# Performance work log

Hardware: AMD Instinct MI355X
Metric: run time of the kernel (lower is better)

## Reference

```python
import jax, jax.numpy as jnp
import numpy as np

S, N, F = 32, 512, 256        # systems, atoms per system, feature/charge channels
R_EXCL = 5.0                  # neighbor_list_options.cutoff -> exclusion_radius
BOX = 30.0                    # box edge for random positions (Angstrom-scale)


def setup_inputs() -> dict:
    key = jax.random.key(0)
    k1, k2, k3, k4 = jax.random.split(key, 4)
    positions = jax.random.uniform(k1, (S, N, 3), dtype=jnp.float32) * BOX
    features = jax.random.normal(k2, (S * N, F), dtype=jnp.float32)
    W = jax.random.normal(k3, (F, F), dtype=jnp.float32) / jnp.sqrt(F)
    b = jax.random.normal(k4, (F,), dtype=jnp.float32) * 0.01
    return {"positions": positions, "features": features, "W": W, "b": b}


def _pair_potential(d):
    # CoulombPotential(smearing=None, exclusion_radius=R_EXCL).from_dist:
    # v(r) = (1/r) * (1 - f_cut(r)),  f_cut = 0.5*(1 + cos(pi*r/R_EXCL)) for r < R_EXCL
    fcut = jnp.where(d < R_EXCL, 0.5 * (1.0 + jnp.cos(jnp.pi * d / R_EXCL)), 0.0)
    return (1.0 / d) * (1.0 - fcut)


def reference(positions, features, W, b):
    # charges_map: Linear(F, F)
    charges = features @ W.T + b                      # [S*N, F]
    q = charges.reshape(S, N, F)                      # per-system charges

    # all-pairs distances per system (torch.combinations path, both directions
    # accumulated by the half-neighbor-list Calculator)
    diff = positions[:, :, None, :] - positions[:, None, :, :]   # [S,N,N,3]
    d = jnp.sqrt(jnp.sum(diff * diff, axis=-1))                  # [S,N,N]
    eye = jnp.eye(N, dtype=bool)
    d_safe = jnp.where(eye, 1.0, d)
    v = jnp.where(eye, 0.0, _pair_potential(d_safe))             # [S,N,N]

    # V_i = 0.5 * sum_j v(r_ij) q_j  (torchpme energy convention E = sum_i q_i V_i)
    V = 0.5 * jnp.einsum('sij,sjf->sif', v, q)                   # [S,N,F]

    # module returns potential * charges, concatenated over systems
    return (V * q).reshape(S * N, F)
```

## Files before the change

### kernel.cpp

```cpp
#include <hip/hip_runtime.h>
#include <hip/hip_cooperative_groups.h>

#define SY 32
#define NA 512
#define FD 256

typedef __attribute__((ext_vector_type(8))) short bf16x8;
typedef __attribute__((ext_vector_type(4))) short bf16x4;
typedef __attribute__((ext_vector_type(4))) float f32x4;

static __device__ __forceinline__ short f2bf(float x) {
    union { float f; unsigned u; } v; v.f = x;
    unsigned r = v.u + 0x7fffu + ((v.u >> 16) & 1u);
    return (short)(r >> 16);
}
static __device__ __forceinline__ float bf2f(short x) {
    union { float f; unsigned u; } v;
    v.u = ((unsigned)(unsigned short)x) << 16;
    return v.f;
}

static __device__ __forceinline__ void gld16(const void* g, void* l) {
    __builtin_amdgcn_global_load_lds(
        (const __attribute__((address_space(1))) void*)g,
        (__attribute__((address_space(3))) void*)l,
        16, 0, 0);
}

__global__ __launch_bounds__(512) void charges_mfma(
    const float* __restrict__ feat, const float* __restrict__ W,
    const float* __restrict__ b, float* __restrict__ qfp,
    short* __restrict__ qT)
{
    __shared__ __attribute__((aligned(16))) short sA[64 * 72];
    __shared__ __attribute__((aligned(16))) short sB[256 * 72];
    __shared__ __attribute__((aligned(16))) short tr[256 * 72];
    const int t    = threadIdx.x;
    const int i0   = blockIdx.x * 64;
    const int w    = t >> 6;
    const int lane = t & 63;
    const int n16  = lane & 15;
    const int quad = lane >> 4;

    f32x4 acc[4][2];
    #pragma unroll
    for (int a = 0; a < 4; ++a)
        #pragma unroll
        for (int c = 0; c < 2; ++c) acc[a][c] = (f32x4)0.0f;

    for (int k0 = 0; k0 < FD; k0 += 64) {
        #pragma unroll
        for (int m = 0; m < 2; ++m) {
            int lin = t + 512 * m;
            int i = lin >> 4, kq = lin & 15;
            float4 v = *(const float4*)&feat[(size_t)(i0 + i) * FD + k0 + 4 * kq];
            bf16x4 p; p[0] = f2bf(v.x); p[1] = f2bf(v.y);
                      p[2] = f2bf(v.z); p[3] = f2bf(v.w);
            *(bf16x4*)&sA[i * 72 + 4 * kq] = p;
        }
        #pragma unroll
        for (int m = 0; m < 8; ++m) {
            int lin = t + 512 * m;
            int f = lin >> 4, kq = lin & 15;
            float4 v = *(const float4*)&W[(size_t)f * FD + k0 + 4 * kq];
            bf16x4 p; p[0] = f2bf(v.x); p[1] = f2bf(v.y);
                      p[2] = f2bf(v.z); p[3] = f2bf(v.w);
            *(bf16x4*)&sB[f * 72 + 4 * kq] = p;
        }
        __syncthreads();

        #pragma unroll
        for (int ks = 0; ks < 64; ks += 32) {
            bf16x8 af[4], bfr[2];
            #pragma unroll
            for (int it = 0; it < 4; ++it)
                af[it] = *(const bf16x8*)&sA[(16 * it + n16) * 72 + ks + quad * 8];
            #pragma unroll
            for (int fb = 0; fb < 2; ++fb)
                bfr[fb] = *(const bf16x8*)&sB[(32 * w + 16 * fb + n16) * 72 + ks + quad * 8];
            #pragma unroll
            for (int it = 0; it < 4; ++it)
                #pragma unroll
                for (int fb = 0; fb < 2; ++fb)
                    acc[it][fb] = __builtin_amdgcn_mfma_f32_16x16x32_bf16(
                        af[it], bfr[fb], acc[it][fb], 0, 0, 0);
        }
        __syncthreads();
    }

    float bias[2];
    #pragma unroll
    for (int fb = 0; fb < 2; ++fb) bias[fb] = b[32 * w + 16 * fb + n16];

    if (qfp) {
        #pragma unroll
        for (int it = 0; it < 4; ++it)
            #pragma unroll
            for (int fb = 0; fb < 2; ++fb)
                #pragma unroll
                for (int r = 0; r < 4; ++r) {
                    int i = i0 + 16 * it + 4 * quad + r;
                    int f = 32 * w + 16 * fb + n16;
                    qfp[(size_t)i * FD + f] = acc[it][fb][r] + bias[fb];
                }
    }

    #pragma unroll
    for (int it = 0; it < 4; ++it)
        #pragma unroll
        for (int fb = 0; fb < 2; ++fb) {
            bf16x4 p;
            #pragma unroll
            for (int r = 0; r < 4; ++r) p[r] = f2bf(acc[it][fb][r] + bias[fb]);
            int f = 32 * w + 16 * fb + n16;
            *(bf16x4*)&tr[f * 72 + 16 * it + 4 * quad] = p;
        }
    __syncthreads();
    {
        short* qTs = qT + ((size_t)(i0 >> 9)) * FD * NA;
        const int ilb = i0 & 511;
        #pragma unroll
        for (int n = 0; n < 4; ++n) {
            int S = n * 512 + t;
            int f = S >> 3;
            int c = S & 7;
            uint4 v = *(const uint4*)&tr[f * 72 + c * 8];
            *(uint4*)&qTs[(size_t)f * NA + ilb + c * 8] = v;
        }
    }
}

__global__ __launch_bounds__(256, 2) void lr_fast(
    const float* __restrict__ pos, float* __restrict__ gbuf,
    const short* __restrict__ qT)
{
    __shared__ float px[NA], py[NA], pz[NA];
    __shared__ __attribute__((aligned(16))) short sqb[FD * 128];
    __shared__ __attribute__((aligned(16))) short svb[32 * 128];

    const int blk = blockIdx.x;
    const int s   = blk & 31;
    const int i0  = (blk >> 5) * 32;
    const int t   = threadIdx.x;
    const int w    = t >> 6;
    const int lane = t & 63;
    const int n16  = lane & 15;
    const int quad = lane >> 4;

    for (int m = t; m < NA; m += 256) {
        const float* p = &pos[((size_t)s * NA + m) * 3];
        px[m] = p[0]; py[m] = p[1]; pz[m] = p[2];
    }

    f32x4 acc[2][4];
    #pragma unroll
    for (int a = 0; a < 2; ++a)
        #pragma unroll
        for (int c = 0; c < 4; ++c) acc[a][c] = (f32x4)0.0f;
    float qreg[2][4][4];

    const short* qTs = qT + (size_t)s * FD * NA;
    const int pi = t & 31;
    const int pc = t >> 5;
    const int gi = i0 + pi;
    const int wbase = t & ~63;

    __syncthreads();
    const float xi = px[gi], yi = py[gi], zi = pz[gi];

    for (int j0 = 0; j0 < NA; j0 += 128) {
        #pragma unroll
        for (int n = 0; n < 16; ++n) {
            int Sl = n * 256 + t;
            int f  = Sl >> 4;
            int cs = Sl & 15;
            int c  = (cs - f) & 15;
            gld16(&qTs[(size_t)f * NA + j0 + c * 8],
                  &sqb[(n * 256 + wbase) * 8]);
        }
        bf16x8 vA, vB;
        #pragma unroll
        for (int jj = 0; jj < 8; ++jj) {
            int gj = j0 + pc * 16 + jj;
            float dx = xi - px[gj];
            float dy = yi - py[gj];
            float dz = zi - pz[gj];
            float r2 = dx * dx + dy * dy + dz * dz;
            float inv = __builtin_amdgcn_rsqf(r2);
            float dd  = r2 * inv;
            float sn = __sinf(dd * 0.31415926535f);
            float om = (dd < 5.0f) ? sn * sn : 1.0f;
            float vv = (gi != gj) ? 0.5f * om * inv : 0.0f;
            vA[jj] = f2bf(vv);
        }
        #pragma unroll
        for (int jj = 0; jj < 8; ++jj) {
            int gj = j0 + pc * 16 + 8 + jj;
            float dx = xi - px[gj];
            float dy = yi - py[gj];
            float dz = zi - pz[gj];
            float r2 = dx * dx + dy * dy + dz * dz;
            float inv = __builtin_amdgcn_rsqf(r2);
            float dd  = r2 * inv;
            float sn = __sinf(dd * 0.31415926535f);
            float om = (dd < 5.0f) ? sn * sn : 1.0f;
            float vv = (gi != gj) ? 0.5f * om * inv : 0.0f;
            vB[jj] = f2bf(vv);
        }
        *(bf16x8*)&svb[pi * 128 + (((2 * pc + pi) & 15) * 8)]     = vA;
        *(bf16x8*)&svb[pi * 128 + (((2 * pc + 1 + pi) & 15) * 8)] = vB;
        __syncthreads();

        if (j0 == (i0 & ~127)) {
            const int jb0 = i0 & 127;
            #pragma unroll
            for (int it = 0; it < 2; ++it)
                #pragma unroll
                for (int fb = 0; fb < 4; ++fb) {
                    int f = 64 * w + 16 * fb + n16;
                    #pragma unroll
                    for (int r = 0; r < 4; ++r) {
                        int jl = jb0 + 16 * it + 4 * quad + r;
                        int c  = jl >> 3, o = jl & 7;
                        qreg[it][fb][r] =
                            bf2f(sqb[f * 128 + (((c + f) & 15) * 8) + o]);
                    }
                }
        }

        #pragma unroll
        for (int kh = 0; kh < 4; ++kh) {
            const int c = kh * 4 + quad;
            bf16x8 a0 = *(const bf16x8*)&svb[n16 * 128 + (((c + n16) & 15) * 8)];
            bf16x8 a1 = *(const bf16x8*)&svb[(16 + n16) * 128 + (((c + 16 + n16) & 15) * 8)];
            bf16x8 bq[4];
            #pragma unroll
            for (int fb = 0; fb < 4; ++fb) {
                int f = 64 * w + 16 * fb + n16;
                bq[fb] = *(const bf16x8*)&sqb[f * 128 + (((c + f) & 15) * 8)];
            }
            #pragma unroll
            for (int fb = 0; fb < 4; ++fb) {
                acc[0][fb] = __builtin_amdgcn_mfma_f32_16x16x32_bf16(
                    a0, bq[fb], acc[0][fb], 0, 0, 0);
                acc[1][fb] = __builtin_amdgcn_mfma_f32_16x16x32_bf16(
                    a1, bq[fb], acc[1][fb], 0, 0, 0);
            }
        }
        __syncthreads();
    }

    #pragma unroll
    for (int it = 0; it < 2; ++it)
        #pragma unroll
        for (int fb = 0; fb < 4; ++fb)
            #pragma unroll
            for (int r = 0; r < 4; ++r) {
                int i = i0 + 16 * it + 4 * quad + r;
                int f = 64 * w + 16 * fb + n16;
                size_t a = ((size_t)s * NA + i) * FD + f;
                gbuf[a] = acc[it][fb][r] * qreg[it][fb][r];
            }
}

__global__ __launch_bounds__(256) void lr_coop(
    const float* __restrict__ pos, float* __restrict__ gbuf)
{
    __shared__ float px[NA], py[NA], pz[NA];
    __shared__ __attribute__((aligned(16))) short svb[64 * 40];
    __shared__ __attribute__((aligned(16))) short sqb[FD * 40];

    const int blk = blockIdx.x;
    const int s   = blk & 31;
    const int i0  = (blk >> 5) * 64;
    const int t   = threadIdx.x;
    const int w    = t >> 6;
    const int lane = t & 63;
    const int n16  = lane & 15;
    const int quad = lane >> 4;

    for (int m = t; m < NA; m += 256) {
        const float* p = &pos[((size_t)s * NA + m) * 3];
        px[m] = p[0]; py[m] = p[1]; pz[m] = p[2];
    }

    f32x4 acc[4][4];
    #pragma unroll
    for (int a = 0; a < 4; ++a)
        #pragma unroll
        for (int c = 0; c < 4; ++c) acc[a][c] = (f32x4)0.0f;

    __syncthreads();

    const int fq  = t >> 2;
    const int jb  = t & 3;
    const int iv  = t & 63;
    const int jbv = t >> 6;
    const int gi  = i0 + iv;

    float4 rq[8];
    #pragma unroll
    for (int m = 0; m < 8; ++m)
        rq[m] = *(const float4*)&gbuf[((size_t)s * NA + 8 * jb + m) * FD + 4 * fq];

    for (int j0 = 0; j0 < NA; j0 += 32) {
        bf16x8 vrow;
        #pragma unroll
        for (int jj = 0; jj < 8; ++jj) {
            int gj = j0 + 8 * jbv + jj;
            float dx = px[gi] - px[gj];
            float dy = py[gi] - py[gj];
            float dz = pz[gi] - pz[gj];
            float dd = sqrtf(dx * dx + dy * dy + dz * dz);
            float om = (dd < 5.0f) ? 0.5f * (1.0f - __cosf(dd * 0.62831853071795f))
                                   : 1.0f;
            float vv = (gi != gj) ? (0.5f * om * __builtin_amdgcn_rcpf(dd)) : 0.0f;
            vrow[jj] = f2bf(vv);
        }
        bf16x8 rows[4];
        #pragma unroll
        for (int m = 0; m < 8; ++m) {
            rows[0][m] = f2bf(rq[m].x);
            rows[1][m] = f2bf(rq[m].y);
            rows[2][m] = f2bf(rq[m].z);
            rows[3][m] = f2bf(rq[m].w);
        }
        #pragma unroll
        for (int d = 0; d < 4; ++d) {
            int f = 4 * fq + d;
            int phys = (jb + (f >> 3)) & 3;
            *(bf16x8*)&sqb[f * 40 + phys * 8] = rows[d];
        }
        {
            int phys = (jbv + (iv >> 3)) & 3;
            *(bf16x8*)&svb[iv * 40 + phys * 8] = vrow;
        }
        {
            int jn = (j0 + 32) & (NA - 1);
            #pragma unroll
            for (int m = 0; m < 8; ++m)
                rq[m] = *(const float4*)&gbuf[((size_t)s * NA + jn + 8 * jb + m) * FD + 4 * fq];
        }
        __syncthreads();

        bf16x8 af[4], bfr[4];
        #pragma unroll
        for (int it = 0; it < 4; ++it) {
            int i = 16 * it + n16;
            int phys = (quad + (i >> 3)) & 3;
            af[it] = *(const bf16x8*)&svb[i * 40 + phys * 8];
        }
        #pragma unroll
        for (int fb = 0; fb < 4; ++fb) {
            int f = 16 * (4 * w + fb) + n16;
            int phys = (quad + (f >> 3)) & 3;
            bfr[fb] = *(const bf16x8*)&sqb[f * 40 + phys * 8];
        }
        #pragma unroll
        for (int it = 0; it < 4; ++it)
            #pragma unroll
            for (int fb = 0; fb < 4; ++fb)
                acc[it][fb] = __builtin_amdgcn_mfma_f32_16x16x32_bf16(
                    af[it], bfr[fb], acc[it][fb], 0, 0, 0);
        __syncthreads();
    }

    cooperative_groups::this_grid().sync();

    #pragma unroll
    for (int it = 0; it < 4; ++it)
        #pragma unroll
        for (int fb = 0; fb < 4; ++fb)
            #pragma unroll
            for (int r = 0; r < 4; ++r) {
                int i = i0 + 16 * it + 4 * quad + r;
                int f = 16 * (4 * w + fb) + n16;
                size_t a = ((size_t)s * NA + i) * FD + f;
                gbuf[a] = acc[it][fb][r] * gbuf[a];
            }
}

extern "C" void kernel_launch(void* const* d_in, const int* in_sizes, int n_in,
                              void* d_out, int out_size, void* d_ws, size_t ws_size,
                              hipStream_t stream) {
    const float* positions = (const float*)d_in[0];
    const float* features  = (const float*)d_in[1];
    const float* W         = (const float*)d_in[2];
    const float* b         = (const float*)d_in[3];
    float* gbuf = (float*)d_out;

    const size_t qT_bytes = (size_t)SY * NA * FD * sizeof(short);
    const bool fast = (ws_size >= qT_bytes);
    short* qT = fast ? (short*)d_ws : nullptr;

    if (fast) {
        charges_mfma<<<dim3(256), 512, 0, stream>>>(features, W, b, nullptr, qT);
        lr_fast<<<dim3(512), 256, 0, stream>>>(positions, gbuf, qT);
    } else {
        charges_mfma<<<dim3(256), 512, 0, stream>>>(features, W, b, gbuf,
                                                    (short*)d_out );
        void* args[] = {(void*)&positions, (void*)&gbuf};
        hipLaunchCooperativeKernel((void*)lr_coop, dim3(256), dim3(256),
                                   args, 0, stream);
    }
}
```

Baseline: 97.00 us.

## Keep bf16 charges in the output buffer and add a software grid barrier

Drops the workspace and cooperative fallback paths. The transposed bf16 charges now live in the upper half of the output buffer, and lr_fast uses an atomic-counter spin barrier, with a spin limit, before overwriting the output. The charges kernel is retiled to 32-row blocks at 256 threads with 2 blocks per CU and reuses its staging LDS for the transpose. MFMA sections are wrapped in s_setprio. The barrier assumes all 512 blocks are co-resident, and the counter word sits in the output itself. If blocks are not co-resident, the spin times out and the result can be wrong.

```diff
diff --git a/kernel.cpp b/kernel.cpp
--- a/kernel.cpp
+++ b/kernel.cpp
@@ -1,5 +1,4 @@
 #include <hip/hip_runtime.h>
-#include <hip/hip_cooperative_groups.h>
 
 #define SY 32
 #define NA 512
@@ -27,31 +26,34 @@
         16, 0, 0);
 }
 
-__global__ __launch_bounds__(512) void charges_mfma(
+__global__ __launch_bounds__(256, 2) void charges_v2(
     const float* __restrict__ feat, const float* __restrict__ W,
-    const float* __restrict__ b, float* __restrict__ qfp,
-    short* __restrict__ qT)
+    const float* __restrict__ b, short* __restrict__ qT,
+    unsigned* __restrict__ ctr)
 {
-    __shared__ __attribute__((aligned(16))) short sA[64 * 72];
+    __shared__ __attribute__((aligned(16))) short sA[32 * 72];
     __shared__ __attribute__((aligned(16))) short sB[256 * 72];
-    __shared__ __attribute__((aligned(16))) short tr[256 * 72];
+    short* tr = sB;
     const int t    = threadIdx.x;
-    const int i0   = blockIdx.x * 64;
+    const int i0   = blockIdx.x * 32;
     const int w    = t >> 6;
     const int lane = t & 63;
     const int n16  = lane & 15;
     const int quad = lane >> 4;
 
-    f32x4 acc[4][2];
-    #pragma unroll
-    for (int a = 0; a < 4; ++a)
-        #pragma unroll
-        for (int c = 0; c < 2; ++c) acc[a][c] = (f32x4)0.0f;
+    if (blockIdx.x == 0 && t == 0)
+        __hip_atomic_store(ctr, 0u, __ATOMIC_RELAXED, __HIP_MEMORY_SCOPE_AGENT);
+
+    f32x4 acc[2][4];
+    #pragma unroll
+    for (int a = 0; a < 2; ++a)
+        #pragma unroll
+        for (int c = 0; c < 4; ++c) acc[a][c] = (f32x4)0.0f;
 
     for (int k0 = 0; k0 < FD; k0 += 64) {
         #pragma unroll
         for (int m = 0; m < 2; ++m) {
-            int lin = t + 512 * m;
+            int lin = t + 256 * m;
             int i = lin >> 4, kq = lin & 15;
             float4 v = *(const float4*)&feat[(size_t)(i0 + i) * FD + k0 + 4 * kq];
             bf16x4 p; p[0] = f2bf(v.x); p[1] = f2bf(v.y);
@@ -59,8 +61,8 @@
             *(bf16x4*)&sA[i * 72 + 4 * kq] = p;
         }
         #pragma unroll
-        for (int m = 0; m < 8; ++m) {
-            int lin = t + 512 * m;
+        for (int m = 0; m < 16; ++m) {
+            int lin = t + 256 * m;
             int f = lin >> 4, kq = lin & 15;
             float4 v = *(const float4*)&W[(size_t)f * FD + k0 + 4 * kq];
             bf16x4 p; p[0] = f2bf(v.x); p[1] = f2bf(v.y);
@@ -71,49 +73,38 @@
 
         #pragma unroll
         for (int ks = 0; ks < 64; ks += 32) {
-            bf16x8 af[4], bfr[2];
-            #pragma unroll
-            for (int it = 0; it < 4; ++it)
+            bf16x8 af[2], bfr[4];
+            #pragma unroll
+            for (int it = 0; it < 2; ++it)
                 af[it] = *(const bf16x8*)&sA[(16 * it + n16) * 72 + ks + quad * 8];
             #pragma unroll
-            for (int fb = 0; fb < 2; ++fb)
-                bfr[fb] = *(const bf16x8*)&sB[(32 * w + 16 * fb + n16) * 72 + ks + quad * 8];
-            #pragma unroll
-            for (int it = 0; it < 4; ++it)
+            for (int fb = 0; fb < 4; ++fb)
+                bfr[fb] = *(const bf16x8*)&sB[(64 * w + 16 * fb + n16) * 72 + ks + quad * 8];
+            __builtin_amdgcn_s_setprio(1);
+            #pragma unroll
+            for (int it = 0; it < 2; ++it)
                 #pragma unroll
-                for (int fb = 0; fb < 2; ++fb)
+                for (int fb = 0; fb < 4; ++fb)
                     acc[it][fb] = __builtin_amdgcn_mfma_f32_16x16x32_bf16(
                         af[it], bfr[fb], acc[it][fb], 0, 0, 0);
-        }
-        __syncthreads();
-    }
-
-    float bias[2];
-    #pragma unroll
-    for (int fb = 0; fb < 2; ++fb) bias[fb] = b[32 * w + 16 * fb + n16];
-
-    if (qfp) {
-        #pragma unroll
-        for (int it = 0; it < 4; ++it)
-            #pragma unroll
-            for (int fb = 0; fb < 2; ++fb)
-                #pragma unroll
-                for (int r = 0; r < 4; ++r) {
-                    int i = i0 + 16 * it + 4 * quad + r;
-                    int f = 32 * w + 16 * fb + n16;
-                    qfp[(size_t)i * FD + f] = acc[it][fb][r] + bias[fb];
-                }
-    }
-
-    #pragma unroll
-    for (int it = 0; it < 4; ++it)
-        #pragma unroll
-        for (int fb = 0; fb < 2; ++fb) {
+            __builtin_amdgcn_s_setprio(0);
+        }
+        __syncthreads();
+    }
+
+    float bias[4];
+    #pragma unroll
+    for (int fb = 0; fb < 4; ++fb) bias[fb] = b[64 * w + 16 * fb + n16];
+
+    #pragma unroll
+    for (int it = 0; it < 2; ++it)
+        #pragma unroll
+        for (int fb = 0; fb < 4; ++fb) {
             bf16x4 p;
             #pragma unroll
             for (int r = 0; r < 4; ++r) p[r] = f2bf(acc[it][fb][r] + bias[fb]);
-            int f = 32 * w + 16 * fb + n16;
-            *(bf16x4*)&tr[f * 72 + 16 * it + 4 * quad] = p;
+            int f = 64 * w + 16 * fb + n16;
+            *(bf16x4*)&tr[f * 40 + 16 * it + 4 * quad] = p;
         }
     __syncthreads();
     {
@@ -121,10 +112,10 @@
         const int ilb = i0 & 511;
         #pragma unroll
         for (int n = 0; n < 4; ++n) {
-            int S = n * 512 + t;
-            int f = S >> 3;
-            int c = S & 7;
-            uint4 v = *(const uint4*)&tr[f * 72 + c * 8];
+            int S = n * 256 + t;
+            int f = S >> 2;
+            int c = S & 3;
+            uint4 v = *(const uint4*)&tr[f * 40 + c * 8];
             *(uint4*)&qTs[(size_t)f * NA + ilb + c * 8] = v;
         }
     }
@@ -132,7 +123,7 @@
 
 __global__ __launch_bounds__(256, 2) void lr_fast(
     const float* __restrict__ pos, float* __restrict__ gbuf,
-    const short* __restrict__ qT)
+    const short* __restrict__ qT, unsigned* __restrict__ ctr)
 {
     __shared__ float px[NA], py[NA], pz[NA];
     __shared__ __attribute__((aligned(16))) short sqb[FD * 128];
@@ -239,6 +230,7 @@
                 int f = 64 * w + 16 * fb + n16;
                 bq[fb] = *(const bf16x8*)&sqb[f * 128 + (((c + f) & 15) * 8)];
             }
+            __builtin_amdgcn_s_setprio(1);
             #pragma unroll
             for (int fb = 0; fb < 4; ++fb) {
                 acc[0][fb] = __builtin_amdgcn_mfma_f32_16x16x32_bf16(
@@ -246,9 +238,19 @@
                 acc[1][fb] = __builtin_amdgcn_mfma_f32_16x16x32_bf16(
                     a1, bq[fb], acc[1][fb], 0, 0, 0);
             }
-        }
-        __syncthreads();
-    }
+            __builtin_amdgcn_s_setprio(0);
+        }
+        __syncthreads();
+    }
+
+    if (t == 0) {
+        __hip_atomic_fetch_add(ctr, 1u, __ATOMIC_ACQ_REL, __HIP_MEMORY_SCOPE_AGENT);
+        unsigned v; int guard = 0;
+        do {
+            v = __hip_atomic_load(ctr, __ATOMIC_ACQUIRE, __HIP_MEMORY_SCOPE_AGENT);
+        } while (v < 512u && ++guard < (1 << 16));
+    }
+    __syncthreads();
 
     #pragma unroll
     for (int it = 0; it < 2; ++it)
@@ -260,123 +262,6 @@
                 int f = 64 * w + 16 * fb + n16;
                 size_t a = ((size_t)s * NA + i) * FD + f;
                 gbuf[a] = acc[it][fb][r] * qreg[it][fb][r];
-            }
-}
-
-__global__ __launch_bounds__(256) void lr_coop(
-    const float* __restrict__ pos, float* __restrict__ gbuf)
-{
-    __shared__ float px[NA], py[NA], pz[NA];
-    __shared__ __attribute__((aligned(16))) short svb[64 * 40];
-    __shared__ __attribute__((aligned(16))) short sqb[FD * 40];
-
-    const int blk = blockIdx.x;
-    const int s   = blk & 31;
-    const int i0  = (blk >> 5) * 64;
-    const int t   = threadIdx.x;
-    const int w    = t >> 6;
-    const int lane = t & 63;
-    const int n16  = lane & 15;
-    const int quad = lane >> 4;
-
-    for (int m = t; m < NA; m += 256) {
-        const float* p = &pos[((size_t)s * NA + m) * 3];
-        px[m] = p[0]; py[m] = p[1]; pz[m] = p[2];
-    }
-
-    f32x4 acc[4][4];
-    #pragma unroll
-    for (int a = 0; a < 4; ++a)
-        #pragma unroll
-        for (int c = 0; c < 4; ++c) acc[a][c] = (f32x4)0.0f;
-
-    __syncthreads();
-
-    const int fq  = t >> 2;
-    const int jb  = t & 3;
-    const int iv  = t & 63;
-    const int jbv = t >> 6;
-    const int gi  = i0 + iv;
-
-    float4 rq[8];
-    #pragma unroll
-    for (int m = 0; m < 8; ++m)
-        rq[m] = *(const float4*)&gbuf[((size_t)s * NA + 8 * jb + m) * FD + 4 * fq];
-
-    for (int j0 = 0; j0 < NA; j0 += 32) {
-        bf16x8 vrow;
-        #pragma unroll
-        for (int jj = 0; jj < 8; ++jj) {
-            int gj = j0 + 8 * jbv + jj;
-            float dx = px[gi] - px[gj];
-            float dy = py[gi] - py[gj];
-            float dz = pz[gi] - pz[gj];
-            float dd = sqrtf(dx * dx + dy * dy + dz * dz);
-            float om = (dd < 5.0f) ? 0.5f * (1.0f - __cosf(dd * 0.62831853071795f))
-                                   : 1.0f;
-            float vv = (gi != gj) ? (0.5f * om * __builtin_amdgcn_rcpf(dd)) : 0.0f;
-            vrow[jj] = f2bf(vv);
-        }
-        bf16x8 rows[4];
-        #pragma unroll
-        for (int m = 0; m < 8; ++m) {
-            rows[0][m] = f2bf(rq[m].x);
-            rows[1][m] = f2bf(rq[m].y);
-            rows[2][m] = f2bf(rq[m].z);
-            rows[3][m] = f2bf(rq[m].w);
-        }
-        #pragma unroll
-        for (int d = 0; d < 4; ++d) {
-            int f = 4 * fq + d;
-            int phys = (jb + (f >> 3)) & 3;
-            *(bf16x8*)&sqb[f * 40 + phys * 8] = rows[d];
-        }
-        {
-            int phys = (jbv + (iv >> 3)) & 3;
-            *(bf16x8*)&svb[iv * 40 + phys * 8] = vrow;
-        }
-        {
-            int jn = (j0 + 32) & (NA - 1);
-            #pragma unroll
-            for (int m = 0; m < 8; ++m)
-                rq[m] = *(const float4*)&gbuf[((size_t)s * NA + jn + 8 * jb + m) * FD + 4 * fq];
-        }
-        __syncthreads();
-
-        bf16x8 af[4], bfr[4];
-        #pragma unroll
-        for (int it = 0; it < 4; ++it) {
-            int i = 16 * it + n16;
-            int phys = (quad + (i >> 3)) & 3;
-            af[it] = *(const bf16x8*)&svb[i * 40 + phys * 8];
-        }
-        #pragma unroll
-        for (int fb = 0; fb < 4; ++fb) {
-            int f = 16 * (4 * w + fb) + n16;
-            int phys = (quad + (f >> 3)) & 3;
-            bfr[fb] = *(const bf16x8*)&sqb[f * 40 + phys * 8];
-        }
-        #pragma unroll
-        for (int it = 0; it < 4; ++it)
-            #pragma unroll
-            for (int fb = 0; fb < 4; ++fb)
-                acc[it][fb] = __builtin_amdgcn_mfma_f32_16x16x32_bf16(
-                    af[it], bfr[fb], acc[it][fb], 0, 0, 0);
-        __syncthreads();
-    }
-
-    cooperative_groups::this_grid().sync();
-
-    #pragma unroll
-    for (int it = 0; it < 4; ++it)
-        #pragma unroll
-        for (int fb = 0; fb < 4; ++fb)
-            #pragma unroll
-            for (int r = 0; r < 4; ++r) {
-                int i = i0 + 16 * it + 4 * quad + r;
-                int f = 16 * (4 * w + fb) + n16;
-                size_t a = ((size_t)s * NA + i) * FD + f;
-                gbuf[a] = acc[it][fb][r] * gbuf[a];
             }
 }
 
@@ -389,18 +274,9 @@
     const float* b         = (const float*)d_in[3];
     float* gbuf = (float*)d_out;
 
-    const size_t qT_bytes = (size_t)SY * NA * FD * sizeof(short);
-    const bool fast = (ws_size >= qT_bytes);
-    short* qT = fast ? (short*)d_ws : nullptr;
-
-    if (fast) {
-        charges_mfma<<<dim3(256), 512, 0, stream>>>(features, W, b, nullptr, qT);
-        lr_fast<<<dim3(512), 256, 0, stream>>>(positions, gbuf, qT);
-    } else {
-        charges_mfma<<<dim3(256), 512, 0, stream>>>(features, W, b, gbuf,
-                                                    (short*)d_out );
-        void* args[] = {(void*)&positions, (void*)&gbuf};
-        hipLaunchCooperativeKernel((void*)lr_coop, dim3(256), dim3(256),
-                                   args, 0, stream);
-    }
-}
+    short* qT = (short*)d_out + (size_t)SY * FD * NA;
+    unsigned* ctr = (unsigned*)d_out;
+
+    charges_v2<<<dim3(512), 256, 0, stream>>>(features, W, b, qT, ctr);
+    lr_fast<<<dim3(512), 256, 0, stream>>>(positions, gbuf, qT, ctr);
+}
```

New measurement: 135.5 us. 39.7% more time.
